# Performance work log

Measured on AMD Instinct MI355X. Metric: run time of the kernel, lower is better.

The kernel has to match this reference:

```python
import jax, jax.numpy as jnp
import numpy as np

B, S, E, H = 8, 4096, 1024, 1024


def log_g(x):
    # log(relu(x)+0.5) for x>=0, -softplus(-x) for x<0
    return jnp.where(x >= 0, jnp.log(jax.nn.relu(x) + 0.5), -jax.nn.softplus(-x))


def parallel_scan_log(log_coeffs, log_values):
    # log_coeffs: (B,S,H); log_values: (B,S+1,H)
    a_star = jnp.cumsum(log_coeffs, axis=1)
    a_star = jnp.pad(a_star, ((0, 0), (1, 0), (0, 0)))  # (B,S+1,H)
    log_h0_plus_b_star = jax.lax.cumlogsumexp(log_values - a_star, axis=1)
    log_h = a_star + log_h0_plus_b_star
    return jnp.exp(log_h)[:, 1:]  # (B,S,H)


def setup_inputs() -> dict:
    key = jax.random.key(0)
    ks = jax.random.split(key, 8)
    scale = 1.0 / np.sqrt(E)
    return {
        "x": jax.random.normal(ks[0], (B, S, E), dtype=jnp.float32),
        "h_0": jax.random.uniform(ks[1], (B, 1, H), dtype=jnp.float32),
        "Wz": jax.random.normal(ks[2], (E, H), dtype=jnp.float32) * scale,
        "bz": jnp.zeros((H,), dtype=jnp.float32),
        "Wh": jax.random.normal(ks[3], (E, H), dtype=jnp.float32) * scale,
        "bh": jnp.zeros((H,), dtype=jnp.float32),
        "Wo": jax.random.normal(ks[4], (H, E), dtype=jnp.float32) * scale,
        "bo": jnp.zeros((E,), dtype=jnp.float32),
    }


def reference(x, h_0, Wz, bz, Wh, bh, Wo, bo):
    k = jnp.einsum("bse,eh->bsh", x, Wz) + bz
    log_z = -jax.nn.softplus(-k)
    log_coeffs = -jax.nn.softplus(k)
    log_h_0 = log_g(h_0)                                       # (B,1,H)
    log_tilde_h = log_g(jnp.einsum("bse,eh->bsh", x, Wh) + bh)  # (B,S,H)
    log_values = jnp.concatenate([log_h_0, log_z + log_tilde_h], axis=1)
    h = parallel_scan_log(log_coeffs, log_values)               # (B,S,H)
    out = jnp.einsum("bsh,he->bse", h, Wo) + bo
    return out, h[:, -1:, :]
```

## Files before the change

kernel.cpp:

```cpp
#include <hip/hip_runtime.h>
#include <hip/hip_bf16.h>
#include <cstdint>
#include <cstddef>

static constexpr int Bb   = 8;
static constexpr int Ss   = 4096;
static constexpr int Ee   = 1024;
static constexpr int Hh   = 1024;
static constexpr int Mtot = Bb * Ss;
static constexpr int NCH  = 32;
static constexpr int SCH  = Ss / NCH;

using f32x4 = __attribute__((ext_vector_type(4))) float;
using s16x8 = __attribute__((ext_vector_type(8))) short;
using u16x8 = __attribute__((ext_vector_type(8))) unsigned short;

__device__ __forceinline__ uint16_t f2bf(float f) {
  union { float f; uint32_t u; } c; c.f = f;
  uint32_t u = c.u;
  return (uint16_t)((u + 0x7FFFu + ((u >> 16) & 1u)) >> 16);
}
__device__ __forceinline__ float bf2f(uint32_t lo16) {
  union { uint32_t u; float f; } c; c.u = lo16 << 16;
  return c.f;
}

#define GLOAD_LDS16(gp, lp)                                                  \
  __builtin_amdgcn_global_load_lds(                                          \
      (const __attribute__((address_space(1))) void*)(gp),                   \
      (__attribute__((address_space(3))) void*)(lp), 16, 0, 0)

__global__ void cast_x_kernel(const float* __restrict__ x,
                              uint16_t* __restrict__ xb, int n) {
  int stride = gridDim.x * blockDim.x * 8;
  for (int i = (blockIdx.x * blockDim.x + threadIdx.x) * 8; i < n; i += stride) {
    const float4* p = (const float4*)(x + i);
    float4 v0 = p[0];
    float4 v1 = p[1];
    u16x8 r;
    r[0] = f2bf(v0.x); r[1] = f2bf(v0.y); r[2] = f2bf(v0.z); r[3] = f2bf(v0.w);
    r[4] = f2bf(v1.x); r[5] = f2bf(v1.y); r[6] = f2bf(v1.z); r[7] = f2bf(v1.w);
    *(u16x8*)(xb + i) = r;
  }
}

__global__ void wprep_kernel(const float* __restrict__ Wz,
                             const float* __restrict__ Wh,
                             const float* __restrict__ Wo,
                             uint16_t* __restrict__ Wzt,
                             uint16_t* __restrict__ Wht,
                             uint16_t* __restrict__ Wot) {
  __shared__ float tile[64][65];
  const float* src = (blockIdx.z == 0) ? Wz : (blockIdx.z == 1) ? Wh : Wo;
  uint16_t*    dst = (blockIdx.z == 0) ? Wzt : (blockIdx.z == 1) ? Wht : Wot;
  int k0 = blockIdx.x * 64, n0 = blockIdx.y * 64;
  int t = threadIdx.x;
  int c = t & 63, r0 = t >> 6;
  #pragma unroll
  for (int i = 0; i < 16; i++) {
    int r = r0 + i * 4;
    tile[r][c] = src[(size_t)(k0 + r) * 1024 + n0 + c];
  }
  __syncthreads();
  int k = t & 63, nn0 = t >> 6;
  #pragma unroll
  for (int i = 0; i < 16; i++) {
    int n = nn0 + i * 4;
    dst[(size_t)(n0 + n) * 1024 + k0 + k] = f2bf(tile[k][n]);
  }
}

template <bool DUAL, int NT, int KC>
__global__ __launch_bounds__(256)
void gemm_kernel(const uint16_t* __restrict__ A,
                 const uint16_t* __restrict__ Bt0,
                 const uint16_t* __restrict__ Bt1,
                 const float* __restrict__ bias0,
                 const float* __restrict__ bias1,
                 uint32_t* __restrict__ cv_out,
                 float* __restrict__ out,
                 int NYB, int N) {
  constexpr int NFR = NT / 32;
  __shared__ __align__(16) uint16_t As[128 * 32];
  __shared__ __align__(16) uint16_t Bs0[NT * 32];
  __shared__ __align__(16) uint16_t Bs1[DUAL ? NT * 32 : 8];

  const int cpx = (int)gridDim.x >> 3;
  const int wg  = ((int)blockIdx.x & 7) * cpx + ((int)blockIdx.x >> 3);
  const int yb  = wg % NYB, xb = wg / NYB;

  const int t = threadIdx.x;
  const int lane = t & 63, wid = t >> 6;
  const int wr = wid >> 1, wc = wid & 1;
  const int lr = lane & 15, kg = lane >> 4;
  const int m_base = xb * 128;
  const int n_base = yb * NT;
  const int wcN = wc * (NT / 2);

  const int srow = lane >> 2;
  const int scol = (lane & 3) * 8;
  const uint16_t* pA  = A   + (size_t)(m_base + wid * 16 + srow) * KC + scol;
  const uint16_t* pB0 = Bt0 + (size_t)(n_base + wid * 16 + srow) * KC + scol;
  const uint16_t* pB1 =
      DUAL ? (Bt1 + (size_t)(n_base + wid * 16 + srow) * KC + scol) : nullptr;
  char* lA  = (char*)As  + wid * 1024;
  char* lB0 = (char*)Bs0 + wid * 1024;
  char* lB1 = (char*)Bs1 + wid * 1024;

  f32x4 zero = {0.f, 0.f, 0.f, 0.f};
  f32x4 acc0[4][NFR];
  f32x4 acc1[DUAL ? 4 : 1][NFR];
  #pragma unroll
  for (int i = 0; i < 4; i++)
    #pragma unroll
    for (int j = 0; j < NFR; j++) acc0[i][j] = zero;
  if constexpr (DUAL) {
    #pragma unroll
    for (int i = 0; i < 4; i++)
      #pragma unroll
      for (int j = 0; j < NFR; j++) acc1[i][j] = zero;
  }

  #pragma unroll 8
  for (int k0 = 0; k0 < KC; k0 += 32) {
    GLOAD_LDS16(pA + k0, lA);
    GLOAD_LDS16(pA + (size_t)64 * KC + k0, lA + 4096);
    GLOAD_LDS16(pB0 + k0, lB0);
    if constexpr (NT == 128)
      GLOAD_LDS16(pB0 + (size_t)64 * KC + k0, lB0 + 4096);
    if constexpr (DUAL) {
      GLOAD_LDS16(pB1 + k0, lB1);
      if constexpr (NT == 128)
        GLOAD_LDS16(pB1 + (size_t)64 * KC + k0, lB1 + 4096);
    }
    __syncthreads();

    s16x8 af[4], b0f[NFR], b1f[NFR];
    #pragma unroll
    for (int mf = 0; mf < 4; mf++)
      af[mf] = *(const s16x8*)(As + (wr * 64 + mf * 16 + lr) * 32 + kg * 8);
    #pragma unroll
    for (int nf = 0; nf < NFR; nf++) {
      b0f[nf] = *(const s16x8*)(Bs0 + (wcN + nf * 16 + lr) * 32 + kg * 8);
      if constexpr (DUAL)
        b1f[nf] = *(const s16x8*)(Bs1 + (wcN + nf * 16 + lr) * 32 + kg * 8);
    }
    #pragma unroll
    for (int mf = 0; mf < 4; mf++)
      #pragma unroll
      for (int nf = 0; nf < NFR; nf++) {
        acc0[mf][nf] = __builtin_amdgcn_mfma_f32_16x16x32_bf16(
            af[mf], b0f[nf], acc0[mf][nf], 0, 0, 0);
        if constexpr (DUAL)
          acc1[mf][nf] = __builtin_amdgcn_mfma_f32_16x16x32_bf16(
              af[mf], b1f[nf], acc1[mf][nf], 0, 0, 0);
      }
    __syncthreads();
  }

  #pragma unroll
  for (int mf = 0; mf < 4; mf++) {
    #pragma unroll
    for (int nf = 0; nf < NFR; nf++) {
      #pragma unroll
      for (int j = 0; j < 4; j++) {
        int row = m_base + wr * 64 + mf * 16 + kg * 4 + j;
        int col = n_base + wcN + nf * 16 + lr;
        if constexpr (DUAL) {
          float kv = acc0[mf][nf][j] + bias0[col];
          float av = acc1[mf][nf][j] + bias1[col];
          float ek = __expf(-kv);
          float zf = 1.f / (1.f + ek);
          float cf = ek * zf;
          float gf = (av >= 0.f) ? (av + 0.5f)
                                 : (1.f / (1.f + __expf(-av)));
          float vf = zf * gf;
          cv_out[(size_t)row * N + col] =
              (uint32_t)f2bf(cf) | ((uint32_t)f2bf(vf) << 16);
        } else {
          out[(size_t)row * N + col] = acc0[mf][nf][j] + bias0[col];
        }
      }
    }
  }
  (void)pB1; (void)bias1; (void)cv_out; (void)out;
}

__global__ void scan1_kernel(const uint32_t* __restrict__ cv,
                             float* __restrict__ Cc, float* __restrict__ Vc) {
  int h = blockIdx.x * 256 + threadIdx.x;
  int j = blockIdx.y, b = blockIdx.z;
  size_t base = ((size_t)b * Ss + (size_t)j * SCH) * Hh + h;
  float C = 1.f, V = 0.f;
  #pragma unroll 4
  for (int s = 0; s < SCH; s++) {
    uint32_t p = cv[base + (size_t)s * Hh];
    float c = bf2f(p & 0xFFFFu), v = bf2f(p >> 16);
    C *= c;
    V = fmaf(c, V, v);
  }
  size_t o = ((size_t)b * NCH + j) * Hh + h;
  Cc[o] = C;
  Vc[o] = V;
}

__global__ void scan2_kernel(const float* __restrict__ h0,
                             const float* __restrict__ Cc,
                             const float* __restrict__ Vc,
                             float* __restrict__ hinit,
                             float* __restrict__ hlast) {
  int idx = blockIdx.x * 256 + threadIdx.x;
  float x = h0[idx];
  float st = (x >= 0.f) ? (x + 0.5f) : (1.f / (1.f + __expf(-x)));
  int b = idx >> 10, h = idx & 1023;
  for (int j = 0; j < NCH; j++) {
    size_t o = ((size_t)b * NCH + j) * Hh + h;
    hinit[o] = st;
    st = fmaf(Cc[o], st, Vc[o]);
  }
  hlast[idx] = st;
}

__global__ void scan3_kernel(const uint32_t* __restrict__ cv,
                             const float* __restrict__ hinit,
                             uint16_t* __restrict__ hb) {
  int h = blockIdx.x * 256 + threadIdx.x;
  int j = blockIdx.y, b = blockIdx.z;
  size_t base = ((size_t)b * Ss + (size_t)j * SCH) * Hh + h;
  float st = hinit[((size_t)b * NCH + j) * Hh + h];
  #pragma unroll 4
  for (int s = 0; s < SCH; s++) {
    uint32_t p = cv[base + (size_t)s * Hh];
    st = fmaf(bf2f(p & 0xFFFFu), st, bf2f(p >> 16));
    hb[base + (size_t)s * Hh] = f2bf(st);
  }
}

extern "C" void kernel_launch(void* const* d_in, const int* in_sizes, int n_in,
                              void* d_out, int out_size, void* d_ws, size_t ws_size,
                              hipStream_t stream) {
  const float* x  = (const float*)d_in[0];
  const float* h0 = (const float*)d_in[1];
  const float* Wz = (const float*)d_in[2];
  const float* bz = (const float*)d_in[3];
  const float* Wh = (const float*)d_in[4];
  const float* bh = (const float*)d_in[5];
  const float* Wo = (const float*)d_in[6];
  const float* bo = (const float*)d_in[7];
  float* out = (float*)d_out;

  uint32_t* cv = (uint32_t*)d_out;

  char* p = (char*)d_ws;
  uint16_t* xb  = (uint16_t*)p; p += (size_t)Mtot * Ee * 2;
  uint16_t* Wzt = (uint16_t*)p; p += (size_t)Ee * Hh * 2;
  uint16_t* Wht = (uint16_t*)p; p += (size_t)Ee * Hh * 2;
  uint16_t* Wot = (uint16_t*)p; p += (size_t)Hh * Ee * 2;
  float* Cc     = (float*)p;    p += (size_t)Bb * NCH * Hh * 4;
  float* Vc     = (float*)p;    p += (size_t)Bb * NCH * Hh * 4;
  float* hinit  = (float*)p;    p += (size_t)Bb * NCH * Hh * 4;
  uint16_t* hb  = (uint16_t*)p; p += (size_t)Mtot * Hh * 2;

  hipLaunchKernelGGL(cast_x_kernel, dim3(2048), dim3(256), 0, stream,
                     x, xb, Mtot * Ee);
  hipLaunchKernelGGL(wprep_kernel, dim3(16, 16, 3), dim3(256), 0, stream,
                     Wz, Wh, Wo, Wzt, Wht, Wot);
  hipLaunchKernelGGL((gemm_kernel<true, 64, 1024>),
                     dim3((Mtot / 128) * (Hh / 64)), dim3(256), 0, stream,
                     xb, Wzt, Wht, bz, bh, cv, (float*)nullptr,
                     Hh / 64, Hh);
  hipLaunchKernelGGL(scan1_kernel, dim3(Hh / 256, NCH, Bb), dim3(256), 0, stream,
                     cv, Cc, Vc);
  hipLaunchKernelGGL(scan2_kernel, dim3((Bb * Hh) / 256), dim3(256), 0, stream,
                     h0, Cc, Vc, hinit, out + (size_t)Mtot * Ee);
  hipLaunchKernelGGL(scan3_kernel, dim3(Hh / 256, NCH, Bb), dim3(256), 0, stream,
                     cv, hinit, hb);
  hipLaunchKernelGGL((gemm_kernel<false, 128, 1024>),
                     dim3((Mtot / 128) * (Ee / 128)), dim3(256), 0, stream,
                     hb, Wot, (const uint16_t*)nullptr, bo,
                     (const float*)nullptr, (uint32_t*)nullptr, out,
                     Ee / 128, Ee);
}
```

Baseline: 575.4 us.

## Fuse chunk-summary scan into gate GEMM epilogue and vectorize scan3

Removes the separate scan1 pass. The dual gate GEMM epilogue now builds the per-chunk (C, V) affine summary for its 128-row tile, which matches one scan chunk. It does this with a per-thread fold, cross-lane shuffles and a small LDS combine across the two row waves. This avoids re-reading the whole packed coefficient/value buffer from memory and saves one launch. scan3 now handles two hidden columns per thread with 64-bit loads and 32-bit stores. One side effect is that the summaries are built from unrounded fp32 gates rather than their bf16-rounded values, so they differ slightly from what scan3 replays.

```diff
diff --git a/kernel.cpp b/kernel.cpp
--- a/kernel.cpp
+++ b/kernel.cpp
@@ -79,11 +79,14 @@
                  const float* __restrict__ bias1,
                  uint32_t* __restrict__ cv_out,
                  float* __restrict__ out,
+                 float* __restrict__ Cc,
+                 float* __restrict__ Vc,
                  int NYB, int N) {
   constexpr int NFR = NT / 32;
   __shared__ __align__(16) uint16_t As[128 * 32];
   __shared__ __align__(16) uint16_t Bs0[NT * 32];
   __shared__ __align__(16) uint16_t Bs1[DUAL ? NT * 32 : 8];
+  __shared__ float CompLds[DUAL ? 256 : 1];
 
   const int cpx = (int)gridDim.x >> 3;
   const int wg  = ((int)blockIdx.x & 7) * cpx + ((int)blockIdx.x >> 3);
@@ -158,15 +161,17 @@
     __syncthreads();
   }
 
-  #pragma unroll
-  for (int mf = 0; mf < 4; mf++) {
-    #pragma unroll
-    for (int nf = 0; nf < NFR; nf++) {
-      #pragma unroll
-      for (int j = 0; j < 4; j++) {
-        int row = m_base + wr * 64 + mf * 16 + kg * 4 + j;
-        int col = n_base + wcN + nf * 16 + lr;
-        if constexpr (DUAL) {
+  if constexpr (DUAL) {
+    float Cw[2] = {1.f, 1.f}, Vw[2] = {0.f, 0.f};
+    #pragma unroll
+    for (int mf = 0; mf < 4; mf++) {
+      #pragma unroll
+      for (int nf = 0; nf < 2; nf++) {
+        float Cs = 1.f, Vs = 0.f;
+        #pragma unroll
+        for (int j = 0; j < 4; j++) {
+          int row = m_base + wr * 64 + mf * 16 + kg * 4 + j;
+          int col = n_base + wcN + nf * 16 + lr;
           float kv = acc0[mf][nf][j] + bias0[col];
           float av = acc1[mf][nf][j] + bias1[col];
           float ek = __expf(-kv);
@@ -177,31 +182,63 @@
           float vf = zf * gf;
           cv_out[(size_t)row * N + col] =
               (uint32_t)f2bf(cf) | ((uint32_t)f2bf(vf) << 16);
-        } else {
+          Vs = fmaf(cf, Vs, vf);
+          Cs *= cf;
+        }
+        {
+          float Co = __shfl_xor(Cs, 16), Vo = __shfl_xor(Vs, 16);
+          bool later = (kg & 1) != 0;
+          float CA = later ? Co : Cs, VA = later ? Vo : Vs;
+          float CB = later ? Cs : Co, VB = later ? Vs : Vo;
+          Cs = CA * CB; Vs = fmaf(CB, VA, VB);
+        }
+        {
+          float Co = __shfl_xor(Cs, 32), Vo = __shfl_xor(Vs, 32);
+          bool later = (kg & 2) != 0;
+          float CA = later ? Co : Cs, VA = later ? Vo : Vs;
+          float CB = later ? Cs : Co, VB = later ? Vs : Vo;
+          Cs = CA * CB; Vs = fmaf(CB, VA, VB);
+        }
+        Vw[nf] = fmaf(Cs, Vw[nf], Vs);
+        Cw[nf] = Cw[nf] * Cs;
+      }
+    }
+    if (kg == 0) {
+      #pragma unroll
+      for (int nf = 0; nf < 2; nf++) {
+        int idx = ((((wr * 2 + wc) * 2 + nf) * 16) + lr) * 2;
+        CompLds[idx] = Cw[nf];
+        CompLds[idx + 1] = Vw[nf];
+      }
+    }
+    __syncthreads();
+    if (wid == 0) {
+      int wc2 = lane >> 5, nf2 = (lane >> 4) & 1, lr2 = lane & 15;
+      int i0 = ((((0 * 2 + wc2) * 2 + nf2) * 16) + lr2) * 2;
+      int i1 = ((((1 * 2 + wc2) * 2 + nf2) * 16) + lr2) * 2;
+      float C0 = CompLds[i0], V0 = CompLds[i0 + 1];
+      float C1 = CompLds[i1], V1 = CompLds[i1 + 1];
+      float C = C0 * C1, V = fmaf(C1, V0, V1);
+      int col = n_base + wc2 * 32 + nf2 * 16 + lr2;
+      size_t o = (size_t)xb * (size_t)N + col;
+      Cc[o] = C;
+      Vc[o] = V;
+    }
+  } else {
+    #pragma unroll
+    for (int mf = 0; mf < 4; mf++) {
+      #pragma unroll
+      for (int nf = 0; nf < NFR; nf++) {
+        #pragma unroll
+        for (int j = 0; j < 4; j++) {
+          int row = m_base + wr * 64 + mf * 16 + kg * 4 + j;
+          int col = n_base + wcN + nf * 16 + lr;
           out[(size_t)row * N + col] = acc0[mf][nf][j] + bias0[col];
         }
       }
     }
   }
-  (void)pB1; (void)bias1; (void)cv_out; (void)out;
-}
-
-__global__ void scan1_kernel(const uint32_t* __restrict__ cv,
-                             float* __restrict__ Cc, float* __restrict__ Vc) {
-  int h = blockIdx.x * 256 + threadIdx.x;
-  int j = blockIdx.y, b = blockIdx.z;
-  size_t base = ((size_t)b * Ss + (size_t)j * SCH) * Hh + h;
-  float C = 1.f, V = 0.f;
-  #pragma unroll 4
-  for (int s = 0; s < SCH; s++) {
-    uint32_t p = cv[base + (size_t)s * Hh];
-    float c = bf2f(p & 0xFFFFu), v = bf2f(p >> 16);
-    C *= c;
-    V = fmaf(c, V, v);
-  }
-  size_t o = ((size_t)b * NCH + j) * Hh + h;
-  Cc[o] = C;
-  Vc[o] = V;
+  (void)pB1; (void)bias1; (void)cv_out; (void)out; (void)Cc; (void)Vc;
 }
 
 __global__ void scan2_kernel(const float* __restrict__ h0,
@@ -224,15 +261,21 @@
 __global__ void scan3_kernel(const uint32_t* __restrict__ cv,
                              const float* __restrict__ hinit,
                              uint16_t* __restrict__ hb) {
-  int h = blockIdx.x * 256 + threadIdx.x;
+  int h2 = (blockIdx.x * 256 + threadIdx.x) * 2;
   int j = blockIdx.y, b = blockIdx.z;
-  size_t base = ((size_t)b * Ss + (size_t)j * SCH) * Hh + h;
-  float st = hinit[((size_t)b * NCH + j) * Hh + h];
+  size_t base = ((size_t)b * Ss + (size_t)j * SCH) * Hh + h2;
+  size_t io = ((size_t)b * NCH + j) * Hh + h2;
+  float2 hi = *(const float2*)(hinit + io);
+  float st0 = hi.x, st1 = hi.y;
   #pragma unroll 4
   for (int s = 0; s < SCH; s++) {
-    uint32_t p = cv[base + (size_t)s * Hh];
-    st = fmaf(bf2f(p & 0xFFFFu), st, bf2f(p >> 16));
-    hb[base + (size_t)s * Hh] = f2bf(st);
+    uint2 p = *(const uint2*)(cv + base + (size_t)s * Hh);
+    st0 = fmaf(bf2f(p.x & 0xFFFFu), st0, bf2f(p.x >> 16));
+    st1 = fmaf(bf2f(p.y & 0xFFFFu), st1, bf2f(p.y >> 16));
+    ushort2 o;
+    o.x = f2bf(st0);
+    o.y = f2bf(st1);
+    *(ushort2*)(hb + base + (size_t)s * Hh) = o;
   }
 }
 
@@ -268,16 +311,14 @@
   hipLaunchKernelGGL((gemm_kernel<true, 64, 1024>),
                      dim3((Mtot / 128) * (Hh / 64)), dim3(256), 0, stream,
                      xb, Wzt, Wht, bz, bh, cv, (float*)nullptr,
-                     Hh / 64, Hh);
-  hipLaunchKernelGGL(scan1_kernel, dim3(Hh / 256, NCH, Bb), dim3(256), 0, stream,
-                     cv, Cc, Vc);
+                     Cc, Vc, Hh / 64, Hh);
   hipLaunchKernelGGL(scan2_kernel, dim3((Bb * Hh) / 256), dim3(256), 0, stream,
                      h0, Cc, Vc, hinit, out + (size_t)Mtot * Ee);
-  hipLaunchKernelGGL(scan3_kernel, dim3(Hh / 256, NCH, Bb), dim3(256), 0, stream,
+  hipLaunchKernelGGL(scan3_kernel, dim3(Hh / 512, NCH, Bb), dim3(256), 0, stream,
                      cv, hinit, hb);
   hipLaunchKernelGGL((gemm_kernel<false, 128, 1024>),
                      dim3((Mtot / 128) * (Ee / 128)), dim3(256), 0, stream,
                      hb, Wot, (const uint16_t*)nullptr, bo,
                      (const float*)nullptr, (uint32_t*)nullptr, out,
-                     Ee / 128, Ee);
-}
+                     (float*)nullptr, (float*)nullptr, Ee / 128, Ee);
+}
```

Measured after the change: 563.6 us. 1.02x faster.
